# Kernel optimization log

Hardware: AMD Instinct MI355X
Metric: run time of the kernel (lower is better)

The kernel has to match this reference:

```python
import jax, jax.numpy as jnp
import numpy as np

N, F_IN, H1, H2, HEADS, E = 8192, 512, 128, 64, 3, 262144
NEG_SLOPE = 0.2  # PyG GATConv default negative_slope


def _add_self_loops(src, dst, n):
    loop = jnp.arange(n, dtype=src.dtype)
    return jnp.concatenate([src, loop]), jnp.concatenate([dst, loop])


def _gcn_conv(x, src, dst, W, b, n):
    # PyG GCNConv: h = x @ W, add self-loops, symmetric D^-1/2 A D^-1/2 aggregation, + bias
    h = x @ W
    s, d = _add_self_loops(src, dst, n)
    deg = jax.ops.segment_sum(jnp.ones(s.shape, h.dtype), d, num_segments=n)
    dinv = jnp.where(deg > 0, jax.lax.rsqrt(deg), 0.0)
    norm = dinv[s] * dinv[d]  # [E']
    return jax.ops.segment_sum(h[s] * norm[:, None], d, num_segments=n) + b


def _gat_conv(x, src, dst, W, a_src, a_dst, b, n, heads, concat):
    # PyG GATConv: per-head linear, LeakyReLU attention logits, segment softmax over
    # incoming edges per destination node, weighted scatter-aggregate.
    out_dim = W.shape[1] // heads
    h = (x @ W).reshape(n, heads, out_dim)  # [N, H, D]
    s, d = _add_self_loops(src, dst, n)
    a_s = jnp.einsum('nhd,hd->nh', h, a_src)
    a_d = jnp.einsum('nhd,hd->nh', h, a_dst)
    e = jax.nn.leaky_relu(a_s[s] + a_d[d], NEG_SLOPE)  # [E', H]
    m = jax.ops.segment_max(e, d, num_segments=n)      # stable softmax per dst segment
    ex = jnp.exp(e - m[d])
    den = jax.ops.segment_sum(ex, d, num_segments=n)
    msg = h[s] * (ex / den[d])[..., None]              # [E', H, D]
    out = jax.ops.segment_sum(msg, d, num_segments=n)  # [N, H, D]
    if concat:
        return out.reshape(n, heads * out_dim) + b
    return out.mean(axis=1) + b


def _forward(x, edge_index, gcn_W1, gcn_b1, gcn_Wmu, gcn_bmu, gcn_Wlv, gcn_blv,
             gat_W1, gat_as1, gat_ad1, gat_b1,
             gat_Wmu, gat_asmu, gat_admu, gat_bmu,
             gat_Wlv, gat_aslv, gat_adlv, gat_blv,
             eps_gcn, eps_gat):
    src, dst = edge_index[0], edge_index[1]
    n = x.shape[0]
    mu_g = lv_g = z_g = None
    for i in range(gcn_W1.shape[0]):  # gcn branches
        h = jax.nn.relu(_gcn_conv(x, src, dst, gcn_W1[i], gcn_b1[i], n))
        mu = _gcn_conv(h, src, dst, gcn_Wmu[i], gcn_bmu[i], n)
        lv = _gcn_conv(h, src, dst, gcn_Wlv[i], gcn_blv[i], n)
        z = mu + eps_gcn[i] * jnp.exp(lv)  # faithful: logvar passed as logstd
        mu_g = mu if mu_g is None else jnp.maximum(mu_g, mu)
        lv_g = lv if lv_g is None else jnp.maximum(lv_g, lv)
        z_g = z if z_g is None else jnp.maximum(z_g, z)
    mu_a = lv_a = z_a = None
    for i in range(gat_W1.shape[0]):  # gat branches
        h = jax.nn.relu(_gat_conv(x, src, dst, gat_W1[i], gat_as1[i], gat_ad1[i], gat_b1[i], n, HEADS, True))
        mu = _gat_conv(h, src, dst, gat_Wmu[i], gat_asmu[i], gat_admu[i], gat_bmu[i], n, HEADS, False)
        lv = _gat_conv(h, src, dst, gat_Wlv[i], gat_aslv[i], gat_adlv[i], gat_blv[i], n, HEADS, False)
        z = mu + eps_gat[i] * jnp.exp(lv)
        mu_a = mu if mu_a is None else jnp.maximum(mu_a, mu)
        lv_a = lv if lv_a is None else jnp.maximum(lv_a, lv)
        z_a = z if z_a is None else jnp.maximum(z_a, z)
    mu_max = jnp.maximum(mu_g, mu_a)
    lv_max = jnp.maximum(lv_g, lv_a)
    z_max = jnp.maximum(z_g, z_a)
    adj = jax.nn.sigmoid(z_max @ z_max.T)  # InnerProductDecoder.forward_all(sigmoid=True)
    return adj, mu_max, lv_max


def setup_inputs():
    key = jax.random.key(0)
    ki = iter(jax.random.split(key, 32))
    p = lambda shape: jax.random.normal(next(ki), shape, dtype=jnp.float32) * 0.05
    x = jax.random.normal(next(ki), (N, F_IN), dtype=jnp.float32)
    edge_index = jax.random.randint(next(ki), (2, E), 0, N)
    return dict(
        x=x, edge_index=edge_index,
        gcn_W1=p((2, F_IN, H1)), gcn_b1=p((2, H1)),
        gcn_Wmu=p((2, H1, H2)), gcn_bmu=p((2, H2)),
        gcn_Wlv=p((2, H1, H2)), gcn_blv=p((2, H2)),
        gat_W1=p((2, F_IN, HEADS * H1)), gat_as1=p((2, HEADS, H1)),
        gat_ad1=p((2, HEADS, H1)), gat_b1=p((2, HEADS * H1)),
        gat_Wmu=p((2, HEADS * H1, HEADS * H2)), gat_asmu=p((2, HEADS, H2)),
        gat_admu=p((2, HEADS, H2)), gat_bmu=p((2, H2)),
        gat_Wlv=p((2, HEADS * H1, HEADS * H2)), gat_aslv=p((2, HEADS, H2)),
        gat_adlv=p((2, HEADS, H2)), gat_blv=p((2, H2)),
        eps_gcn=jax.random.normal(next(ki), (2, N, H2), dtype=jnp.float32),
        eps_gat=jax.random.normal(next(ki), (2, N, H2), dtype=jnp.float32),
    )


def reference(x, edge_index, gcn_W1, gcn_b1, gcn_Wmu, gcn_bmu, gcn_Wlv, gcn_blv,
              gat_W1, gat_as1, gat_ad1, gat_b1,
              gat_Wmu, gat_asmu, gat_admu, gat_bmu,
              gat_Wlv, gat_aslv, gat_adlv, gat_blv,
              eps_gcn, eps_gat):
    return _forward(x, edge_index, gcn_W1, gcn_b1, gcn_Wmu, gcn_bmu, gcn_Wlv, gcn_blv,
                    gat_W1, gat_as1, gat_ad1, gat_b1,
                    gat_Wmu, gat_asmu, gat_admu, gat_bmu,
                    gat_Wlv, gat_aslv, gat_adlv, gat_blv,
                    eps_gcn, eps_gat)
```

## Files before the change

kernel.cpp:

```cpp
#include <hip/hip_runtime.h>
#include <hip/hip_bf16.h>
#include <math.h>
#include <stddef.h>

#define NN 8192
#define NEG_SLOPE 0.2f

typedef _Float16 h8 __attribute__((ext_vector_type(8)));
typedef __attribute__((ext_vector_type(4))) float f32x4;

__device__ __forceinline__ float lrelu(float x) { return x > 0.f ? x : NEG_SLOPE * x; }
__device__ __forceinline__ float sigf(float x) { return 1.f / (1.f + __expf(-x)); }

__device__ __forceinline__ unsigned short f16b(float x) {
    _Float16 h = (_Float16)x;
    unsigned short u;
    __builtin_memcpy(&u, &h, 2);
    return u;
}
__device__ __forceinline__ float f16f(unsigned short u) {
    _Float16 h;
    __builtin_memcpy(&h, &u, 2);
    return (float)h;
}
__device__ __forceinline__ void splith(float x, unsigned short& hu, unsigned short& lu) {
    _Float16 h = (_Float16)x;
    float hf = (float)h;
    _Float16 l = (_Float16)(x - hf);
    __builtin_memcpy(&hu, &h, 2);
    __builtin_memcpy(&lu, &l, 2);
}
__device__ __forceinline__ float2 unpkh(unsigned int v) {
    float2 r;
    r.x = f16f((unsigned short)(v & 0xffffu));
    r.y = f16f((unsigned short)(v >> 16));
    return r;
}
__device__ __forceinline__ unsigned int packh(float a, float b) {
    return (unsigned int)f16b(a) | ((unsigned int)f16b(b) << 16);
}

__device__ __forceinline__ void gll16(const unsigned short* g, unsigned short* l) {
    __builtin_amdgcn_global_load_lds(
        (const __attribute__((address_space(1))) unsigned int*)g,
        (__attribute__((address_space(3))) unsigned int*)l, 16, 0, 0);
}

__global__ void k_zero(int* __restrict__ p, int n) {
    int i = blockIdx.x * blockDim.x + threadIdx.x;
    if (i < n) p[i] = 0;
}
__global__ void k_count(const int* __restrict__ dst, int* __restrict__ cnt, int E) {
    int i = blockIdx.x * blockDim.x + threadIdx.x;
    if (i < E) atomicAdd(&cnt[dst[i]], 1);
}
__global__ void k_dinv(const int* __restrict__ cnt, float* __restrict__ dinv) {
    int i = blockIdx.x * blockDim.x + threadIdx.x;
    if (i < NN) dinv[i] = rsqrtf((float)(cnt[i] + 1));
}
__global__ void k_scan(const int* __restrict__ cnt, int* __restrict__ row_ptr) {
    __shared__ int part[1024];
    int t = threadIdx.x;
    int base = t * 8;
    int loc[8];
    int s = 0;
    #pragma unroll
    for (int j = 0; j < 8; ++j) { loc[j] = s; s += cnt[base + j]; }
    part[t] = s;
    __syncthreads();
    for (int off = 1; off < 1024; off <<= 1) {
        int v = (t >= off) ? part[t - off] : 0;
        __syncthreads();
        part[t] += v;
        __syncthreads();
    }
    int pre = (t == 0) ? 0 : part[t - 1];
    #pragma unroll
    for (int j = 0; j < 8; ++j) row_ptr[base + j] = pre + loc[j];
    if (t == 1023) row_ptr[NN] = part[1023];
}
__global__ void k_fill(const int* __restrict__ src, const int* __restrict__ dst,
                       const int* __restrict__ row_ptr, int* __restrict__ cursor,
                       int* __restrict__ csr_src, int E) {
    int i = blockIdx.x * blockDim.x + threadIdx.x;
    if (i < E) {
        int d = dst[i];
        csr_src[row_ptr[d] + atomicAdd(&cursor[d], 1)] = src[i];
    }
}

__global__ void k_cvt_x(const float* __restrict__ x, unsigned short* __restrict__ xh) {
    int i = blockIdx.x * 256 + threadIdx.x;
    int m = i >> 7, k4 = (i & 127) * 4;
    float4 v = *(const float4*)(x + (size_t)m * 512 + k4);
    ushort4 o;
    o.x = f16b(v.x); o.y = f16b(v.y); o.z = f16b(v.z); o.w = f16b(v.w);
    *(ushort4*)&xh[(size_t)m * 512 + k4] = o;
}

__global__ void k_wT(const float* __restrict__ W, unsigned short* __restrict__ Wt,
                     int K, int N, size_t wt_z_stride, int noff, int noff_z) {
    int b = blockIdx.z;
    W += (size_t)b * K * N;
    Wt += (size_t)b * wt_z_stride;
    int rowbase = noff + b * noff_z;
    int k0 = blockIdx.x * 32, n0 = blockIdx.y * 32;
    __shared__ float tl[32][33];
    int tid = threadIdx.x;
    int r = tid >> 5, cc = tid & 31;
    #pragma unroll
    for (int c = 0; c < 4; ++c)
        tl[r + c * 8][cc] = W[(size_t)(k0 + r + c * 8) * N + n0 + cc];
    __syncthreads();
    #pragma unroll
    for (int c = 0; c < 4; ++c) {
        int n = r + c * 8, k = cc;
        Wt[(size_t)(rowbase + n0 + n) * K + k0 + k] = f16b(tl[k][n]);
    }
}

template <int ROWS>
__device__ __forceinline__ void stage(const unsigned short* __restrict__ gbase, int lda,
                                      unsigned short* lds, int wid, int lane) {
    #pragma unroll
    for (int c = 0; c < ROWS / 32; ++c) {
        int chunk = c * 4 + wid;
        int row = chunk * 8 + (lane >> 3);
        int g = (lane & 7) ^ (row & 7);
        gll16(gbase + (size_t)row * lda + g * 8, lds + chunk * 512);
    }
}
__device__ __forceinline__ h8 fragrh(const unsigned short* lds, int row, int kg) {
    return *(const h8*)(lds + row * 64 + ((kg ^ (row & 7)) * 8));
}

template <int TERMS, int EPI>
__global__ __launch_bounds__(256) void k_gemm2(
    const unsigned short* __restrict__ A2, size_t azs, int lda,
    const unsigned short* __restrict__ B2, size_t bzs, int ldb,
    void* __restrict__ Cv, size_t czs, int ldc, int K) {
    __shared__ __align__(16) unsigned short sAh[128 * 64];
    __shared__ __align__(16) unsigned short sBh[64 * 64];
    __shared__ __align__(16) unsigned short sAl[(TERMS >= 2) ? 128 * 64 : 8];
    __shared__ __align__(16) unsigned short sBl[(TERMS >= 3) ? 64 * 64 : 8];
    const int tid = threadIdx.x;
    const int wid = tid >> 6, lane = tid & 63;
    const int wr = wid >> 1, wc = wid & 1;
    const int lr = lane & 15, lg = lane >> 4;
    const int m0 = blockIdx.x * 128, n0 = blockIdx.y * 64;
    const int z = blockIdx.z;
    A2 += (size_t)z * azs;
    B2 += (size_t)z * bzs;

    const f32x4 zero4 = {0.f, 0.f, 0.f, 0.f};
    f32x4 acc[4][2];
    #pragma unroll
    for (int m = 0; m < 4; ++m)
        #pragma unroll
        for (int n = 0; n < 2; ++n) acc[m][n] = zero4;

    for (int k0 = 0; k0 < K; k0 += 64) {
        stage<128>(A2 + (size_t)m0 * lda + k0, lda, sAh, wid, lane);
        stage<64> (B2 + (size_t)n0 * ldb + k0, ldb, sBh, wid, lane);
        if (TERMS >= 2) stage<128>(A2 + (size_t)m0 * lda + K + k0, lda, sAl, wid, lane);
        if (TERMS >= 3) stage<64> (B2 + (size_t)n0 * ldb + K + k0, ldb, sBl, wid, lane);
        __syncthreads();
        #pragma unroll
        for (int ks = 0; ks < 2; ++ks) {
            const int kg = ks * 4 + lg;
            h8 ah[4], al[4], bh[2], bl[2];
            #pragma unroll
            for (int m = 0; m < 4; ++m) {
                int row = wr * 64 + m * 16 + lr;
                ah[m] = fragrh(sAh, row, kg);
                if (TERMS >= 2) al[m] = fragrh(sAl, row, kg);
            }
            #pragma unroll
            for (int n = 0; n < 2; ++n) {
                int row = wc * 32 + n * 16 + lr;
                bh[n] = fragrh(sBh, row, kg);
                if (TERMS >= 3) bl[n] = fragrh(sBl, row, kg);
            }
            #pragma unroll
            for (int m = 0; m < 4; ++m)
                #pragma unroll
                for (int n = 0; n < 2; ++n) {
                    acc[m][n] = __builtin_amdgcn_mfma_f32_16x16x32_f16(ah[m], bh[n], acc[m][n], 0, 0, 0);
                    if (TERMS >= 2)
                        acc[m][n] = __builtin_amdgcn_mfma_f32_16x16x32_f16(al[m], bh[n], acc[m][n], 0, 0, 0);
                    if (TERMS >= 3)
                        acc[m][n] = __builtin_amdgcn_mfma_f32_16x16x32_f16(ah[m], bl[n], acc[m][n], 0, 0, 0);
                }
        }
        __syncthreads();
    }
    #pragma unroll
    for (int m = 0; m < 4; ++m)
        #pragma unroll
        for (int n = 0; n < 2; ++n)
            #pragma unroll
            for (int j = 0; j < 4; ++j) {
                int row = m0 + wr * 64 + m * 16 + lg * 4 + j;
                int col = n0 + wc * 32 + n * 16 + lr;
                float o = acc[m][n][j];
                if (EPI == 1) {
                    ((float*)Cv + (size_t)z * czs)[(size_t)row * ldc + col] = sigf(o);
                } else if (EPI == 2) {
                    ((unsigned short*)Cv + (size_t)z * czs)[(size_t)row * ldc + col] = f16b(o);
                } else {
                    ((float*)Cv + (size_t)z * czs)[(size_t)row * ldc + col] = o;
                }
            }
}

__global__ void k_gcn_a1(const uint2* __restrict__ xw2, const float* __restrict__ dinv,
                         const int* __restrict__ rp, const int* __restrict__ cs,
                         const float* __restrict__ b1, uint2* __restrict__ hb2) {
    int d = blockIdx.x;
    int t = threadIdx.x;
    float dd = dinv[d];
    uint2 sv = xw2[(size_t)d * 64 + t];
    float2 s0 = unpkh(sv.x), s1 = unpkh(sv.y);
    float a0 = dd * s0.x, a1 = dd * s0.y, a2 = dd * s1.x, a3 = dd * s1.y;
    int e0 = rp[d], e1 = rp[d + 1];
    int j = e0;
    for (; j + 4 <= e1; j += 4) {
        int i0 = cs[j], i1 = cs[j + 1], i2 = cs[j + 2], i3 = cs[j + 3];
        float w0 = dinv[i0], w1 = dinv[i1], w2 = dinv[i2], w3 = dinv[i3];
        uint2 v0 = xw2[(size_t)i0 * 64 + t];
        uint2 v1 = xw2[(size_t)i1 * 64 + t];
        uint2 v2 = xw2[(size_t)i2 * 64 + t];
        uint2 v3 = xw2[(size_t)i3 * 64 + t];
        float2 p;
        p = unpkh(v0.x); a0 += w0 * p.x; a1 += w0 * p.y;
        p = unpkh(v0.y); a2 += w0 * p.x; a3 += w0 * p.y;
        p = unpkh(v1.x); a0 += w1 * p.x; a1 += w1 * p.y;
        p = unpkh(v1.y); a2 += w1 * p.x; a3 += w1 * p.y;
        p = unpkh(v2.x); a0 += w2 * p.x; a1 += w2 * p.y;
        p = unpkh(v2.y); a2 += w2 * p.x; a3 += w2 * p.y;
        p = unpkh(v3.x); a0 += w3 * p.x; a1 += w3 * p.y;
        p = unpkh(v3.y); a2 += w3 * p.x; a3 += w3 * p.y;
    }
    for (; j < e1; ++j) {
        int s = cs[j];
        float w = dinv[s];
        uint2 v = xw2[(size_t)s * 64 + t];
        float2 p;
        p = unpkh(v.x); a0 += w * p.x; a1 += w * p.y;
        p = unpkh(v.y); a2 += w * p.x; a3 += w * p.y;
    }
    int c = 4 * t;
    float o0 = fmaxf(dd * a0 + b1[c], 0.f);
    float o1 = fmaxf(dd * a1 + b1[c + 1], 0.f);
    float o2 = fmaxf(dd * a2 + b1[c + 2], 0.f);
    float o3 = fmaxf(dd * a3 + b1[c + 3], 0.f);
    uint2 o;
    o.x = packh(o0, o1);
    o.y = packh(o2, o3);
    hb2[(size_t)d * 64 + t] = o;
}

__global__ void k_gcn_a2(const uint2* __restrict__ hb2, const float* __restrict__ dinv,
                         const int* __restrict__ rp, const int* __restrict__ cs,
                         uint2* __restrict__ hA2) {
    int d = blockIdx.x;
    int t = threadIdx.x;
    float dd = dinv[d];
    uint2 sv = hb2[(size_t)d * 64 + t];
    float2 s0 = unpkh(sv.x), s1 = unpkh(sv.y);
    float a0 = dd * s0.x, a1 = dd * s0.y, a2 = dd * s1.x, a3 = dd * s1.y;
    int e0 = rp[d], e1 = rp[d + 1];
    int j = e0;
    for (; j + 4 <= e1; j += 4) {
        int i0 = cs[j], i1 = cs[j + 1], i2 = cs[j + 2], i3 = cs[j + 3];
        float w0 = dinv[i0], w1 = dinv[i1], w2 = dinv[i2], w3 = dinv[i3];
        uint2 v0 = hb2[(size_t)i0 * 64 + t];
        uint2 v1 = hb2[(size_t)i1 * 64 + t];
        uint2 v2 = hb2[(size_t)i2 * 64 + t];
        uint2 v3 = hb2[(size_t)i3 * 64 + t];
        float2 p;
        p = unpkh(v0.x); a0 += w0 * p.x; a1 += w0 * p.y;
        p = unpkh(v0.y); a2 += w0 * p.x; a3 += w0 * p.y;
        p = unpkh(v1.x); a0 += w1 * p.x; a1 += w1 * p.y;
        p = unpkh(v1.y); a2 += w1 * p.x; a3 += w1 * p.y;
        p = unpkh(v2.x); a0 += w2 * p.x; a1 += w2 * p.y;
        p = unpkh(v2.y); a2 += w2 * p.x; a3 += w2 * p.y;
        p = unpkh(v3.x); a0 += w3 * p.x; a1 += w3 * p.y;
        p = unpkh(v3.y); a2 += w3 * p.x; a3 += w3 * p.y;
    }
    for (; j < e1; ++j) {
        int s = cs[j];
        float w = dinv[s];
        uint2 v = hb2[(size_t)s * 64 + t];
        float2 p;
        p = unpkh(v.x); a0 += w * p.x; a1 += w * p.y;
        p = unpkh(v.y); a2 += w * p.x; a3 += w * p.y;
    }
    uint2 o;
    o.x = packh(dd * a0, dd * a1);
    o.y = packh(dd * a2, dd * a3);
    hA2[(size_t)d * 64 + t] = o;
}

__global__ void k_gat_log1(const unsigned int* __restrict__ xwu, const float* __restrict__ a_s,
                           const float* __restrict__ a_d, float* __restrict__ as_n,
                           float* __restrict__ ad_n) {
    int br = blockIdx.z;
    int n = blockIdx.x;
    int hd = threadIdx.x >> 6, lane = threadIdx.x & 63;
    const unsigned int* hp = xwu + (size_t)n * 384 + br * 192 + hd * 64;
    const float* av = a_s + br * 384 + hd * 128;
    const float* dv = a_d + br * 384 + hd * 128;
    float2 f = unpkh(hp[lane]);
    float ss = f.x * av[2 * lane] + f.y * av[2 * lane + 1];
    float sd = f.x * dv[2 * lane] + f.y * dv[2 * lane + 1];
    #pragma unroll
    for (int off = 32; off; off >>= 1) {
        ss += __shfl_down(ss, off);
        sd += __shfl_down(sd, off);
    }
    if (lane == 0) {
        as_n[(size_t)br * NN * 3 + n * 3 + hd] = ss;
        ad_n[(size_t)br * NN * 3 + n * 3 + hd] = sd;
    }
}

__global__ void k_gat_log2(const unsigned short* __restrict__ h2gb, const float* __restrict__ asmu,
                           const float* __restrict__ aslv, const float* __restrict__ admu,
                           const float* __restrict__ adlv, float* __restrict__ as_n,
                           float* __restrict__ ad_n) {
    int zz = blockIdx.z;
    int br = zz >> 1, mt = zz & 1;
    int n = blockIdx.x;
    int hd = threadIdx.x >> 6, lane = threadIdx.x & 63;
    const unsigned short* hp = h2gb + (size_t)br * NN * 384 + (size_t)n * 384 + mt * 192 + hd * 64;
    const float* av = (mt ? aslv : asmu) + br * 192 + hd * 64;
    const float* dv = (mt ? adlv : admu) + br * 192 + hd * 64;
    float hv = f16f(hp[lane]);
    float ss = hv * av[lane];
    float sd = hv * dv[lane];
    #pragma unroll
    for (int off = 32; off; off >>= 1) {
        ss += __shfl_down(ss, off);
        sd += __shfl_down(sd, off);
    }
    if (lane == 0) {
        as_n[(size_t)zz * NN * 3 + n * 3 + hd] = ss;
        ad_n[(size_t)zz * NN * 3 + n * 3 + hd] = sd;
    }
}

__global__ void k_gat_attn(const float* __restrict__ as_n, const float* __restrict__ ad_n,
                           const int* __restrict__ rp, const int* __restrict__ cs,
                           float* __restrict__ w_csr, float* __restrict__ w_self, int E3) {
    int zz = blockIdx.z;
    as_n += (size_t)zz * NN * 3;
    ad_n += (size_t)zz * NN * 3;
    w_csr += (size_t)zz * E3;
    w_self += (size_t)zz * NN * 3;
    int d = blockIdx.x;
    int hd = threadIdx.x >> 6, lane = threadIdx.x & 63;
    int e0 = rp[d], e1 = rp[d + 1];
    float add = ad_n[d * 3 + hd];
    float eself = lrelu(as_n[d * 3 + hd] + add);
    float mx = eself;
    for (int j = e0 + lane; j < e1; j += 64) {
        float e = lrelu(as_n[cs[j] * 3 + hd] + add);
        w_csr[(size_t)j * 3 + hd] = e;
        mx = fmaxf(mx, e);
    }
    #pragma unroll
    for (int off = 32; off; off >>= 1) mx = fmaxf(mx, __shfl_xor(mx, off));
    float sm = (lane == 0) ? __expf(eself - mx) : 0.f;
    for (int j = e0 + lane; j < e1; j += 64)
        sm += __expf(w_csr[(size_t)j * 3 + hd] - mx);
    #pragma unroll
    for (int off = 32; off; off >>= 1) sm += __shfl_xor(sm, off);
    float inv = 1.f / sm;
    if (lane == 0) w_self[d * 3 + hd] = __expf(eself - mx) * inv;
    for (int j = e0 + lane; j < e1; j += 64)
        w_csr[(size_t)j * 3 + hd] = __expf(w_csr[(size_t)j * 3 + hd] - mx) * inv;
}

__global__ void k_gat_agg1(const uint2* __restrict__ xw2, const float* __restrict__ w_csr,
                           const float* __restrict__ w_self, const int* __restrict__ rp,
                           const int* __restrict__ cs, const float* __restrict__ b1,
                           uint2* __restrict__ h1s2, int E3) {
    int d = blockIdx.x;
    int t = threadIdx.x;
    int br = t >= 96 ? 1 : 0;
    int c = 4 * t - br * 384;
    int hd = c >> 7;
    const float* wc = w_csr + (size_t)br * E3;
    float ws = w_self[(size_t)br * NN * 3 + d * 3 + hd];
    uint2 sv = xw2[(size_t)d * 192 + t];
    float2 s0 = unpkh(sv.x), s1 = unpkh(sv.y);
    float a0 = ws * s0.x, a1 = ws * s0.y, a2 = ws * s1.x, a3 = ws * s1.y;
    int e0 = rp[d], e1 = rp[d + 1];
    int j = e0;
    for (; j + 4 <= e1; j += 4) {
        int i0 = cs[j], i1 = cs[j + 1], i2 = cs[j + 2], i3 = cs[j + 3];
        float w0 = wc[(size_t)(j + 0) * 3 + hd];
        float w1 = wc[(size_t)(j + 1) * 3 + hd];
        float w2 = wc[(size_t)(j + 2) * 3 + hd];
        float w3 = wc[(size_t)(j + 3) * 3 + hd];
        uint2 v0 = xw2[(size_t)i0 * 192 + t];
        uint2 v1 = xw2[(size_t)i1 * 192 + t];
        uint2 v2 = xw2[(size_t)i2 * 192 + t];
        uint2 v3 = xw2[(size_t)i3 * 192 + t];
        float2 p;
        p = unpkh(v0.x); a0 += w0 * p.x; a1 += w0 * p.y;
        p = unpkh(v0.y); a2 += w0 * p.x; a3 += w0 * p.y;
        p = unpkh(v1.x); a0 += w1 * p.x; a1 += w1 * p.y;
        p = unpkh(v1.y); a2 += w1 * p.x; a3 += w1 * p.y;
        p = unpkh(v2.x); a0 += w2 * p.x; a1 += w2 * p.y;
        p = unpkh(v2.y); a2 += w2 * p.x; a3 += w2 * p.y;
        p = unpkh(v3.x); a0 += w3 * p.x; a1 += w3 * p.y;
        p = unpkh(v3.y); a2 += w3 * p.x; a3 += w3 * p.y;
    }
    for (; j < e1; ++j) {
        int s = cs[j];
        float w = wc[(size_t)j * 3 + hd];
        uint2 v = xw2[(size_t)s * 192 + t];
        float2 p;
        p = unpkh(v.x); a0 += w * p.x; a1 += w * p.y;
        p = unpkh(v.y); a2 += w * p.x; a3 += w * p.y;
    }
    int cg = 4 * t;
    float o0 = fmaxf(a0 + b1[cg], 0.f);
    float o1 = fmaxf(a1 + b1[cg + 1], 0.f);
    float o2 = fmaxf(a2 + b1[cg + 2], 0.f);
    float o3 = fmaxf(a3 + b1[cg + 3], 0.f);
    uint2 o;
    o.x = packh(o0, o1);
    o.y = packh(o2, o3);
    h1s2[(size_t)d * 192 + t] = o;
}

__global__ void k_gat_agg2(const uint2* __restrict__ h2g2, const float* __restrict__ w_csr,
                           const float* __restrict__ w_self, const int* __restrict__ rp,
                           const int* __restrict__ cs, const float* __restrict__ bmu,
                           const float* __restrict__ blv, float* __restrict__ mt_gat, int E3) {
    int d = blockIdx.x;
    int t = threadIdx.x;
    int br = t >= 96 ? 1 : 0;
    int tb = t - br * 96;
    int mt = tb >= 48 ? 1 : 0;
    int c = 4 * tb - mt * 192;
    int hd = c >> 6;
    const float* wc = w_csr + (size_t)(br * 2 + mt) * E3;
    float ws = w_self[(size_t)(br * 2 + mt) * NN * 3 + d * 3 + hd];
    const uint2* hp = h2g2 + (size_t)br * NN * 96;
    uint2 sv = hp[(size_t)d * 96 + tb];
    float2 s0 = unpkh(sv.x), s1 = unpkh(sv.y);
    float a0 = ws * s0.x, a1 = ws * s0.y, a2 = ws * s1.x, a3 = ws * s1.y;
    int e0 = rp[d], e1 = rp[d + 1];
    int j = e0;
    for (; j + 4 <= e1; j += 4) {
        int i0 = cs[j], i1 = cs[j + 1], i2 = cs[j + 2], i3 = cs[j + 3];
        float w0 = wc[(size_t)(j + 0) * 3 + hd];
        float w1 = wc[(size_t)(j + 1) * 3 + hd];
        float w2 = wc[(size_t)(j + 2) * 3 + hd];
        float w3 = wc[(size_t)(j + 3) * 3 + hd];
        uint2 v0 = hp[(size_t)i0 * 96 + tb];
        uint2 v1 = hp[(size_t)i1 * 96 + tb];
        uint2 v2 = hp[(size_t)i2 * 96 + tb];
        uint2 v3 = hp[(size_t)i3 * 96 + tb];
        float2 p;
        p = unpkh(v0.x); a0 += w0 * p.x; a1 += w0 * p.y;
        p = unpkh(v0.y); a2 += w0 * p.x; a3 += w0 * p.y;
        p = unpkh(v1.x); a0 += w1 * p.x; a1 += w1 * p.y;
        p = unpkh(v1.y); a2 += w1 * p.x; a3 += w1 * p.y;
        p = unpkh(v2.x); a0 += w2 * p.x; a1 += w2 * p.y;
        p = unpkh(v2.y); a2 += w2 * p.x; a3 += w2 * p.y;
        p = unpkh(v3.x); a0 += w3 * p.x; a1 += w3 * p.y;
        p = unpkh(v3.y); a2 += w3 * p.x; a3 += w3 * p.y;
    }
    for (; j < e1; ++j) {
        int s = cs[j];
        float w = wc[(size_t)j * 3 + hd];
        uint2 v = hp[(size_t)s * 96 + tb];
        float2 p;
        p = unpkh(v.x); a0 += w * p.x; a1 += w * p.y;
        p = unpkh(v.y); a2 += w * p.x; a3 += w * p.y;
    }
    __shared__ float red[768];
    int rb = br * 384 + mt * 192 + c;
    red[rb] = a0; red[rb + 1] = a1; red[rb + 2] = a2; red[rb + 3] = a3;
    __syncthreads();
    if (t < 128) {
        #pragma unroll
        for (int q = 0; q < 2; ++q) {
            int o = t + q * 128;
            int obr = o >> 7, omt = (o >> 6) & 1, dd = o & 63;
            int base = obr * 384 + omt * 192;
            float tot = red[base + dd] + red[base + 64 + dd] + red[base + 128 + dd];
            const float* bias = omt ? blv : bmu;
            float v = tot * (1.f / 3.f) + bias[obr * 64 + dd];
            mt_gat[((size_t)(obr * 2 + omt) * NN + d) * 64 + dd] = v;
        }
    }
}

__global__ void k_finalize(const float* __restrict__ muv_gcn, const float* __restrict__ gcn_bmu,
                           const float* __restrict__ gcn_blv, const float* __restrict__ mt_gat,
                           const float* __restrict__ eps_gcn, const float* __restrict__ eps_gat,
                           float* __restrict__ mu_o, float* __restrict__ lv_o,
                           unsigned short* __restrict__ z2) {
    int i = blockIdx.x * 256 + threadIdx.x;
    int d = i >> 6, c = i & 63;
    const size_t NN64 = (size_t)NN * 64;
    float mu, lv, zm;
    {
        float m = muv_gcn[(size_t)d * 128 + c] + gcn_bmu[c];
        float l = muv_gcn[(size_t)d * 128 + 64 + c] + gcn_blv[c];
        float z = m + eps_gcn[i] * __expf(l);
        mu = m; lv = l; zm = z;
    }
    {
        float m = muv_gcn[NN64 * 2 + (size_t)d * 128 + c] + gcn_bmu[64 + c];
        float l = muv_gcn[NN64 * 2 + (size_t)d * 128 + 64 + c] + gcn_blv[64 + c];
        float z = m + eps_gcn[NN64 + i] * __expf(l);
        mu = fmaxf(mu, m); lv = fmaxf(lv, l); zm = fmaxf(zm, z);
    }
    #pragma unroll
    for (int br = 0; br < 2; ++br) {
        float m = mt_gat[(size_t)(br * 2 + 0) * NN64 + i];
        float l = mt_gat[(size_t)(br * 2 + 1) * NN64 + i];
        float z = m + eps_gat[(size_t)br * NN64 + i] * __expf(l);
        mu = fmaxf(mu, m); lv = fmaxf(lv, l); zm = fmaxf(zm, z);
    }
    mu_o[i] = mu;
    lv_o[i] = lv;
    unsigned short hh, ll;
    splith(zm, hh, ll);
    z2[(size_t)d * 128 + c] = hh;
    z2[(size_t)d * 128 + 64 + c] = ll;
}

extern "C" void kernel_launch(void* const* d_in, const int* in_sizes, int n_in,
                              void* d_out, int out_size, void* d_ws, size_t ws_size,
                              hipStream_t stream) {
    const float* x  = (const float*)d_in[0];
    const int*   ei = (const int*)d_in[1];
    const int E = in_sizes[1] / 2;
    const int E3 = E * 3;
    const int* src = ei;
    const int* dst = ei + E;

    const float* gcn_W1  = (const float*)d_in[2];
    const float* gcn_b1  = (const float*)d_in[3];
    const float* gcn_Wmu = (const float*)d_in[4];
    const float* gcn_bmu = (const float*)d_in[5];
    const float* gcn_Wlv = (const float*)d_in[6];
    const float* gcn_blv = (const float*)d_in[7];
    const float* gat_W1  = (const float*)d_in[8];
    const float* gat_as1 = (const float*)d_in[9];
    const float* gat_ad1 = (const float*)d_in[10];
    const float* gat_b1  = (const float*)d_in[11];
    const float* gat_Wmu = (const float*)d_in[12];
    const float* gat_asmu= (const float*)d_in[13];
    const float* gat_admu= (const float*)d_in[14];
    const float* gat_bmu = (const float*)d_in[15];
    const float* gat_Wlv = (const float*)d_in[16];
    const float* gat_aslv= (const float*)d_in[17];
    const float* gat_adlv= (const float*)d_in[18];
    const float* gat_blv = (const float*)d_in[19];
    const float* eps_gcn = (const float*)d_in[20];
    const float* eps_gat = (const float*)d_in[21];

    char* p = (char*)d_ws;
    auto alloc = [&](size_t bytes) {
        void* r = (void*)p;
        p += (bytes + 255) & ~(size_t)255;
        return r;
    };
    int*   cnt     = (int*)alloc((size_t)NN * 4);
    int*   cursor  = (int*)alloc((size_t)NN * 4);
    int*   row_ptr = (int*)alloc((size_t)(NN + 1) * 4);
    int*   csr_src = (int*)alloc((size_t)E * 4);
    float* dinv    = (float*)alloc((size_t)NN * 4);
    float* as_n1   = (float*)alloc((size_t)2 * NN * 3 * 4);
    float* ad_n1   = (float*)alloc((size_t)2 * NN * 3 * 4);
    float* wself1  = (float*)alloc((size_t)2 * NN * 3 * 4);
    float* wcsr1   = (float*)alloc((size_t)2 * E3 * 4);
    float* as_n2   = (float*)alloc((size_t)4 * NN * 3 * 4);
    float* ad_n2   = (float*)alloc((size_t)4 * NN * 3 * 4);
    float* wself2  = (float*)alloc((size_t)4 * NN * 3 * 4);
    float* wcsr2   = (float*)alloc((size_t)4 * E3 * 4);
    unsigned short* x2h      = (unsigned short*)alloc((size_t)NN * 512 * 2);
    unsigned short* wt_gcn1  = (unsigned short*)alloc((size_t)256 * 512 * 2);
    unsigned short* wt_gcnmuv= (unsigned short*)alloc((size_t)2 * 128 * 128 * 2);
    unsigned short* wt_gat1  = (unsigned short*)alloc((size_t)768 * 512 * 2);
    unsigned short* wt_gatmuv= (unsigned short*)alloc((size_t)2 * 384 * 384 * 2);
    unsigned short* xwb  = (unsigned short*)alloc((size_t)NN * 768 * 2);
    unsigned short* hb   = (unsigned short*)alloc((size_t)NN * 256 * 2);
    unsigned short* hA   = (unsigned short*)alloc((size_t)NN * 256 * 2);
    float* muv_gcn = (float*)alloc((size_t)2 * NN * 128 * 4);
    unsigned short* h1s  = (unsigned short*)alloc((size_t)NN * 768 * 2);
    unsigned short* h2gb = (unsigned short*)alloc((size_t)2 * NN * 384 * 2);
    float* mt_gat  = (float*)alloc((size_t)4 * NN * 64 * 4);
    unsigned short* z2 = (unsigned short*)alloc((size_t)NN * 128 * 2);

    float* adj  = (float*)d_out;
    float* mu_o = adj + (size_t)NN * NN;
    float* lv_o = mu_o + (size_t)NN * 64;

    k_zero<<<(2 * NN + 255) / 256, 256, 0, stream>>>(cnt, 2 * NN);
    k_count<<<(E + 255) / 256, 256, 0, stream>>>(dst, cnt, E);
    k_dinv<<<(NN + 255) / 256, 256, 0, stream>>>(cnt, dinv);
    k_scan<<<1, 1024, 0, stream>>>(cnt, row_ptr);
    k_fill<<<(E + 255) / 256, 256, 0, stream>>>(src, dst, row_ptr, cursor, csr_src, E);

    k_cvt_x<<<NN * 512 / 4 / 256, 256, 0, stream>>>(x, x2h);
    k_wT<<<dim3(16, 4, 2), 256, 0, stream>>>(gcn_W1, wt_gcn1, 512, 128, 0, 0, 128);
    k_wT<<<dim3(4, 2, 2), 256, 0, stream>>>(gcn_Wmu, wt_gcnmuv, 128, 64, (size_t)128 * 128, 0, 0);
    k_wT<<<dim3(4, 2, 2), 256, 0, stream>>>(gcn_Wlv, wt_gcnmuv, 128, 64, (size_t)128 * 128, 64, 0);
    k_wT<<<dim3(16, 12, 2), 256, 0, stream>>>(gat_W1, wt_gat1, 512, 384, 0, 0, 384);
    k_wT<<<dim3(12, 6, 2), 256, 0, stream>>>(gat_Wmu, wt_gatmuv, 384, 192, (size_t)384 * 384, 0, 0);
    k_wT<<<dim3(12, 6, 2), 256, 0, stream>>>(gat_Wlv, wt_gatmuv, 384, 192, (size_t)384 * 384, 192, 0);

    k_gemm2<1, 2><<<dim3(64, 4, 1), 256, 0, stream>>>(x2h, 0, 512, wt_gcn1, 0, 512,
                                                      xwb, 0, 256, 512);
    k_gcn_a1<<<NN, 64, 0, stream>>>((const uint2*)xwb, dinv, row_ptr, csr_src, gcn_b1,
                                    (uint2*)hb);
    k_gcn_a2<<<NN, 64, 0, stream>>>((const uint2*)hb, dinv, row_ptr, csr_src, (uint2*)hA);
    k_gemm2<1, 0><<<dim3(64, 2, 2), 256, 0, stream>>>(hA, 128, 256, wt_gcnmuv,
                                                      (size_t)128 * 128, 128,
                                                      muv_gcn, (size_t)NN * 128, 128, 128);

    k_gemm2<1, 2><<<dim3(64, 12, 1), 256, 0, stream>>>(x2h, 0, 512, wt_gat1, 0, 512,
                                                       xwb, 0, 768, 512);
    k_gat_log1<<<dim3(NN, 1, 2), 192, 0, stream>>>((const unsigned int*)xwb, gat_as1,
                                                   gat_ad1, as_n1, ad_n1);
    k_gat_attn<<<dim3(NN, 1, 2), 192, 0, stream>>>(as_n1, ad_n1, row_ptr, csr_src,
                                                   wcsr1, wself1, E3);
    k_gat_agg1<<<NN, 192, 0, stream>>>((const uint2*)xwb, wcsr1, wself1, row_ptr, csr_src,
                                       gat_b1, (uint2*)h1s, E3);
    k_gemm2<1, 2><<<dim3(64, 6, 2), 256, 0, stream>>>(h1s, 384, 768, wt_gatmuv,
                                                      (size_t)384 * 384, 384,
                                                      h2gb, (size_t)NN * 384, 384, 384);
    k_gat_log2<<<dim3(NN, 1, 4), 192, 0, stream>>>(h2gb, gat_asmu, gat_aslv, gat_admu,
                                                   gat_adlv, as_n2, ad_n2);
    k_gat_attn<<<dim3(NN, 1, 4), 192, 0, stream>>>(as_n2, ad_n2, row_ptr, csr_src,
                                                   wcsr2, wself2, E3);
    k_gat_agg2<<<NN, 192, 0, stream>>>((const uint2*)h2gb, wcsr2, wself2, row_ptr, csr_src,
                                       gat_bmu, gat_blv, mt_gat, E3);

    k_finalize<<<NN * 64 / 256, 256, 0, stream>>>(muv_gcn, gcn_bmu, gcn_blv, mt_gat,
                                                  eps_gcn, eps_gat, mu_o, lv_o, z2);
    k_gemm2<2, 1><<<dim3(64, 128, 1), 256, 0, stream>>>(z2, 0, 128, z2, 0, 128,
                                                        adj, 0, NN, 64);
}
```

Baseline: 362.3 us.

## Merge setup kernels and unroll gather loops by eight for more loads in flight

Folds the degree-inverse computation into the scan kernel and replaces the zeroing kernel with an async memset. It also merges the mu and logvar weight transposes into one launch per layer. All four aggregation kernels gain an 8-way unrolled gather loop that issues eight neighbour loads before accumulating. The aim is fewer small launches and more memory-level parallelism in the irregular gathers, at the cost of more registers in those kernels.

Measured after the change: 351.7 us. 2.9% less time.

```diff
diff --git a/kernel.cpp b/kernel.cpp
--- a/kernel.cpp
+++ b/kernel.cpp
@@ -46,26 +46,24 @@
         (__attribute__((address_space(3))) unsigned int*)l, 16, 0, 0);
 }
 
-__global__ void k_zero(int* __restrict__ p, int n) {
-    int i = blockIdx.x * blockDim.x + threadIdx.x;
-    if (i < n) p[i] = 0;
-}
 __global__ void k_count(const int* __restrict__ dst, int* __restrict__ cnt, int E) {
     int i = blockIdx.x * blockDim.x + threadIdx.x;
     if (i < E) atomicAdd(&cnt[dst[i]], 1);
 }
-__global__ void k_dinv(const int* __restrict__ cnt, float* __restrict__ dinv) {
-    int i = blockIdx.x * blockDim.x + threadIdx.x;
-    if (i < NN) dinv[i] = rsqrtf((float)(cnt[i] + 1));
-}
-__global__ void k_scan(const int* __restrict__ cnt, int* __restrict__ row_ptr) {
+__global__ void k_scan(const int* __restrict__ cnt, int* __restrict__ row_ptr,
+                       float* __restrict__ dinv) {
     __shared__ int part[1024];
     int t = threadIdx.x;
     int base = t * 8;
     int loc[8];
     int s = 0;
     #pragma unroll
-    for (int j = 0; j < 8; ++j) { loc[j] = s; s += cnt[base + j]; }
+    for (int j = 0; j < 8; ++j) {
+        int cv = cnt[base + j];
+        loc[j] = s;
+        s += cv;
+        dinv[base + j] = rsqrtf((float)(cv + 1));
+    }
     part[t] = s;
     __syncthreads();
     for (int off = 1; off < 1024; off <<= 1) {
@@ -104,6 +102,29 @@
     W += (size_t)b * K * N;
     Wt += (size_t)b * wt_z_stride;
     int rowbase = noff + b * noff_z;
+    int k0 = blockIdx.x * 32, n0 = blockIdx.y * 32;
+    __shared__ float tl[32][33];
+    int tid = threadIdx.x;
+    int r = tid >> 5, cc = tid & 31;
+    #pragma unroll
+    for (int c = 0; c < 4; ++c)
+        tl[r + c * 8][cc] = W[(size_t)(k0 + r + c * 8) * N + n0 + cc];
+    __syncthreads();
+    #pragma unroll
+    for (int c = 0; c < 4; ++c) {
+        int n = r + c * 8, k = cc;
+        Wt[(size_t)(rowbase + n0 + n) * K + k0 + k] = f16b(tl[k][n]);
+    }
+}
+
+__global__ void k_wT2(const float* __restrict__ Wmu, const float* __restrict__ Wlv,
+                      unsigned short* __restrict__ Wt, int K, int N,
+                      size_t wt_br_stride, int lv_rowoff) {
+    int z = blockIdx.z;
+    int mt = z >> 1, b = z & 1;
+    const float* W = (mt ? Wlv : Wmu) + (size_t)b * K * N;
+    Wt += (size_t)b * wt_br_stride;
+    int rowbase = mt ? lv_rowoff : 0;
     int k0 = blockIdx.x * 32, n0 = blockIdx.y * 32;
     __shared__ float tl[32][33];
     int tid = threadIdx.x;
@@ -224,6 +245,21 @@
     float a0 = dd * s0.x, a1 = dd * s0.y, a2 = dd * s1.x, a3 = dd * s1.y;
     int e0 = rp[d], e1 = rp[d + 1];
     int j = e0;
+    for (; j + 8 <= e1; j += 8) {
+        int idx[8]; float w[8]; uint2 v[8];
+        #pragma unroll
+        for (int q = 0; q < 8; ++q) idx[q] = cs[j + q];
+        #pragma unroll
+        for (int q = 0; q < 8; ++q) w[q] = dinv[idx[q]];
+        #pragma unroll
+        for (int q = 0; q < 8; ++q) v[q] = xw2[(size_t)idx[q] * 64 + t];
+        #pragma unroll
+        for (int q = 0; q < 8; ++q) {
+            float2 p;
+            p = unpkh(v[q].x); a0 += w[q] * p.x; a1 += w[q] * p.y;
+            p = unpkh(v[q].y); a2 += w[q] * p.x; a3 += w[q] * p.y;
+        }
+    }
     for (; j + 4 <= e1; j += 4) {
         int i0 = cs[j], i1 = cs[j + 1], i2 = cs[j + 2], i3 = cs[j + 3];
         float w0 = dinv[i0], w1 = dinv[i1], w2 = dinv[i2], w3 = dinv[i3];
@@ -271,6 +307,21 @@
     float a0 = dd * s0.x, a1 = dd * s0.y, a2 = dd * s1.x, a3 = dd * s1.y;
     int e0 = rp[d], e1 = rp[d + 1];
     int j = e0;
+    for (; j + 8 <= e1; j += 8) {
+        int idx[8]; float w[8]; uint2 v[8];
+        #pragma unroll
+        for (int q = 0; q < 8; ++q) idx[q] = cs[j + q];
+        #pragma unroll
+        for (int q = 0; q < 8; ++q) w[q] = dinv[idx[q]];
+        #pragma unroll
+        for (int q = 0; q < 8; ++q) v[q] = hb2[(size_t)idx[q] * 64 + t];
+        #pragma unroll
+        for (int q = 0; q < 8; ++q) {
+            float2 p;
+            p = unpkh(v[q].x); a0 += w[q] * p.x; a1 += w[q] * p.y;
+            p = unpkh(v[q].y); a2 += w[q] * p.x; a3 += w[q] * p.y;
+        }
+    }
     for (; j + 4 <= e1; j += 4) {
         int i0 = cs[j], i1 = cs[j + 1], i2 = cs[j + 2], i3 = cs[j + 3];
         float w0 = dinv[i0], w1 = dinv[i1], w2 = dinv[i2], w3 = dinv[i3];
@@ -398,6 +449,21 @@
     float a0 = ws * s0.x, a1 = ws * s0.y, a2 = ws * s1.x, a3 = ws * s1.y;
     int e0 = rp[d], e1 = rp[d + 1];
     int j = e0;
+    for (; j + 8 <= e1; j += 8) {
+        int idx[8]; float w[8]; uint2 v[8];
+        #pragma unroll
+        for (int q = 0; q < 8; ++q) idx[q] = cs[j + q];
+        #pragma unroll
+        for (int q = 0; q < 8; ++q) w[q] = wc[(size_t)(j + q) * 3 + hd];
+        #pragma unroll
+        for (int q = 0; q < 8; ++q) v[q] = xw2[(size_t)idx[q] * 192 + t];
+        #pragma unroll
+        for (int q = 0; q < 8; ++q) {
+            float2 p;
+            p = unpkh(v[q].x); a0 += w[q] * p.x; a1 += w[q] * p.y;
+            p = unpkh(v[q].y); a2 += w[q] * p.x; a3 += w[q] * p.y;
+        }
+    }
     for (; j + 4 <= e1; j += 4) {
         int i0 = cs[j], i1 = cs[j + 1], i2 = cs[j + 2], i3 = cs[j + 3];
         float w0 = wc[(size_t)(j + 0) * 3 + hd];
@@ -456,6 +522,21 @@
     float a0 = ws * s0.x, a1 = ws * s0.y, a2 = ws * s1.x, a3 = ws * s1.y;
     int e0 = rp[d], e1 = rp[d + 1];
     int j = e0;
+    for (; j + 8 <= e1; j += 8) {
+        int idx[8]; float w[8]; uint2 v[8];
+        #pragma unroll
+        for (int q = 0; q < 8; ++q) idx[q] = cs[j + q];
+        #pragma unroll
+        for (int q = 0; q < 8; ++q) w[q] = wc[(size_t)(j + q) * 3 + hd];
+        #pragma unroll
+        for (int q = 0; q < 8; ++q) v[q] = hp[(size_t)idx[q] * 96 + tb];
+        #pragma unroll
+        for (int q = 0; q < 8; ++q) {
+            float2 p;
+            p = unpkh(v[q].x); a0 += w[q] * p.x; a1 += w[q] * p.y;
+            p = unpkh(v[q].y); a2 += w[q] * p.x; a3 += w[q] * p.y;
+        }
+    }
     for (; j + 4 <= e1; j += 4) {
         int i0 = cs[j], i1 = cs[j + 1], i2 = cs[j + 2], i3 = cs[j + 3];
         float w0 = wc[(size_t)(j + 0) * 3 + hd];
@@ -606,19 +687,18 @@
     float* mu_o = adj + (size_t)NN * NN;
     float* lv_o = mu_o + (size_t)NN * 64;
 
-    k_zero<<<(2 * NN + 255) / 256, 256, 0, stream>>>(cnt, 2 * NN);
+    hipMemsetAsync(cnt, 0, (size_t)2 * NN * 4, stream);
     k_count<<<(E + 255) / 256, 256, 0, stream>>>(dst, cnt, E);
-    k_dinv<<<(NN + 255) / 256, 256, 0, stream>>>(cnt, dinv);
-    k_scan<<<1, 1024, 0, stream>>>(cnt, row_ptr);
+    k_scan<<<1, 1024, 0, stream>>>(cnt, row_ptr, dinv);
     k_fill<<<(E + 255) / 256, 256, 0, stream>>>(src, dst, row_ptr, cursor, csr_src, E);
 
     k_cvt_x<<<NN * 512 / 4 / 256, 256, 0, stream>>>(x, x2h);
     k_wT<<<dim3(16, 4, 2), 256, 0, stream>>>(gcn_W1, wt_gcn1, 512, 128, 0, 0, 128);
-    k_wT<<<dim3(4, 2, 2), 256, 0, stream>>>(gcn_Wmu, wt_gcnmuv, 128, 64, (size_t)128 * 128, 0, 0);
-    k_wT<<<dim3(4, 2, 2), 256, 0, stream>>>(gcn_Wlv, wt_gcnmuv, 128, 64, (size_t)128 * 128, 64, 0);
+    k_wT2<<<dim3(4, 2, 4), 256, 0, stream>>>(gcn_Wmu, gcn_Wlv, wt_gcnmuv, 128, 64,
+                                             (size_t)128 * 128, 64);
     k_wT<<<dim3(16, 12, 2), 256, 0, stream>>>(gat_W1, wt_gat1, 512, 384, 0, 0, 384);
-    k_wT<<<dim3(12, 6, 2), 256, 0, stream>>>(gat_Wmu, wt_gatmuv, 384, 192, (size_t)384 * 384, 0, 0);
-    k_wT<<<dim3(12, 6, 2), 256, 0, stream>>>(gat_Wlv, wt_gatmuv, 384, 192, (size_t)384 * 384, 192, 0);
+    k_wT2<<<dim3(12, 6, 4), 256, 0, stream>>>(gat_Wmu, gat_Wlv, wt_gatmuv, 384, 192,
+                                              (size_t)384 * 384, 192);
 
     k_gemm2<1, 2><<<dim3(64, 4, 1), 256, 0, stream>>>(x2h, 0, 512, wt_gcn1, 0, 512,
                                                       xwb, 0, 256, 512);
```
